# Kernel tuning notes

Hardware: AMD Instinct MI355X
Metric: run time of the kernel (lower is better)

## Reference

```python
import jax, jax.numpy as jnp
import numpy as np

B, S, D = 8, 4096, 512
BLOCK, LEFT, RIGHT = 64, 1, 1
FF = 2048
EPS = 1e-6


def setup_inputs() -> dict:
    key = jax.random.key(0)
    ks = jax.random.split(key, 16)
    sd = 1.0 / np.sqrt(D)
    sf = 1.0 / np.sqrt(FF)
    return {
        "x": jax.random.normal(ks[0], (B, S, D), jnp.float32),
        "Wq": jax.random.normal(ks[1], (D, D), jnp.float32) * sd,
        "bq": jnp.zeros((D,), jnp.float32),
        "Wk": jax.random.normal(ks[2], (D, D), jnp.float32) * sd,
        "bk": jnp.zeros((D,), jnp.float32),
        "Wv": jax.random.normal(ks[3], (D, D), jnp.float32) * sd,
        "bv": jnp.zeros((D,), jnp.float32),
        "W1": jax.random.normal(ks[4], (D, FF), jnp.float32) * sd,
        "b1": jnp.zeros((FF,), jnp.float32),
        "W2": jax.random.normal(ks[5], (FF, D), jnp.float32) * sf,
        "b2": jnp.zeros((D,), jnp.float32),
        "g1": jnp.ones((D,), jnp.float32),
        "be1": jnp.zeros((D,), jnp.float32),
        "g2": jnp.ones((D,), jnp.float32),
        "be2": jnp.zeros((D,), jnp.float32),
    }


def layernorm(x, g, b):
    m = jnp.mean(x, axis=-1, keepdims=True)
    v = jnp.mean(jnp.square(x - m), axis=-1, keepdims=True)
    return g * (x - m) * jax.lax.rsqrt(v + EPS) + b


def local_attention(x, Wq, bq, Wk, bk, Wv, bv):
    Bsz, Sl, Dm = x.shape
    nb = Sl // BLOCK          # number of blocks
    nw = LEFT + RIGHT + 1     # window (in blocks)
    q = (x @ Wq + bq).reshape(Bsz, nb, BLOCK, Dm)
    k = (x @ Wk + bk).reshape(Bsz, nb, BLOCK, Dm)
    v = (x @ Wv + bv).reshape(Bsz, nb, BLOCK, Dm)
    # pad block axis so every query block has LEFT/RIGHT neighbor blocks
    kp = jnp.pad(k, ((0, 0), (LEFT, RIGHT), (0, 0), (0, 0)))
    vp = jnp.pad(v, ((0, 0), (LEFT, RIGHT), (0, 0), (0, 0)))
    # gather windows: (B, nb, nw*BLOCK, D)
    k_win = jnp.stack([kp[:, j:j + nb] for j in range(nw)], axis=2).reshape(Bsz, nb, nw * BLOCK, Dm)
    v_win = jnp.stack([vp[:, j:j + nb] for j in range(nw)], axis=2).reshape(Bsz, nb, nw * BLOCK, Dm)
    # mask out-of-range (padded) blocks at sequence edges
    blk = jnp.arange(nb)[:, None] + jnp.arange(nw)[None, :] - LEFT  # (nb, nw)
    mask = ((blk >= 0) & (blk < nb))
    mask = jnp.repeat(mask, BLOCK, axis=1)  # (nb, nw*BLOCK)
    scores = jnp.einsum('bnqd,bnkd->bnqk', q, k_win) / jnp.sqrt(jnp.float32(Dm))
    scores = jnp.where(mask[None, :, None, :], scores, jnp.float32(-1e9))
    attn = jax.nn.softmax(scores, axis=-1)
    out = jnp.einsum('bnqk,bnkd->bnqd', attn, v_win)
    return out.reshape(Bsz, Sl, Dm)


def reference(x, Wq, bq, Wk, bk, Wv, bv, W1, b1, W2, b2, g1, be1, g2, be2):
    # inference mode: dropout is identity
    a = local_attention(x, Wq, bq, Wk, bk, Wv, bv)
    out1 = layernorm(x + a, g1, be1)
    ffn = jnp.maximum(out1 @ W1 + b1, 0.0) @ W2 + b2
    return layernorm(out1 + ffn, g2, be2)
```

## Files before the change

### kernel.cpp

```cpp
#include <hip/hip_runtime.h>


typedef __bf16 bf16;
typedef __bf16 bf16x8 __attribute__((ext_vector_type(8)));
typedef float  f32x4  __attribute__((ext_vector_type(4)));

#define DEV __device__ __forceinline__

#define BAR()  do { asm volatile("" ::: "memory"); __builtin_amdgcn_s_barrier(); asm volatile("" ::: "memory"); } while (0)
#define WAITV(n) asm volatile("s_waitcnt vmcnt(" #n ")" ::: "memory")
#define WAITV0() asm volatile("s_waitcnt vmcnt(0)" ::: "memory")

DEV void gload_lds16(const void* g, void* lds) {
  __builtin_amdgcn_global_load_lds(
      (const __attribute__((address_space(1))) void*)g,
      (__attribute__((address_space(3))) void*)lds, 16, 0, 0);
}

__global__ __launch_bounds__(256) void cast_to_bf16(const float* __restrict__ in,
                                                    bf16* __restrict__ out, int n8) {
  int i = blockIdx.x * 256 + threadIdx.x;
  if (i >= n8) return;
  float4 a0 = ((const float4*)in)[i * 2];
  float4 a1 = ((const float4*)in)[i * 2 + 1];
  bf16x8 o;
  o[0] = (bf16)a0.x; o[1] = (bf16)a0.y; o[2] = (bf16)a0.z; o[3] = (bf16)a0.w;
  o[4] = (bf16)a1.x; o[5] = (bf16)a1.y; o[6] = (bf16)a1.z; o[7] = (bf16)a1.w;
  ((bf16x8*)out)[i] = o;
}

__global__ __launch_bounds__(256) void transpose_cast(const float* __restrict__ W,
                                                      bf16* __restrict__ Wt, int K, int N) {
  __shared__ bf16 tile[64][66];
  const int n0 = blockIdx.x * 64, k0 = blockIdx.y * 64;
  const int t = threadIdx.x;
#pragma unroll
  for (int it = 0; it < 16; ++it) {
    int c = it * 256 + t;
    int kr = c >> 6, nc = c & 63;
    tile[nc][kr] = (bf16)W[(size_t)(k0 + kr) * N + n0 + nc];
  }
  __syncthreads();
#pragma unroll
  for (int it = 0; it < 2; ++it) {
    int c = it * 256 + t;
    int nr = c >> 3, kg = (c & 7) * 8;
    bf16x8 v;
#pragma unroll
    for (int e = 0; e < 8; ++e) v[e] = tile[nr][kg + e];
    *(bf16x8*)(Wt + (size_t)(n0 + nr) * K + k0 + kg) = v;
  }
}

__global__ __launch_bounds__(256) void concat_bias(const float* __restrict__ bq,
                                                   const float* __restrict__ bk,
                                                   const float* __restrict__ bv,
                                                   float* __restrict__ o) {
  int i = blockIdx.x * 256 + threadIdx.x;
  if (i < 512) o[i] = bq[i];
  else if (i < 1024) o[i] = bk[i - 512];
  else if (i < 1536) o[i] = bv[i - 1024];
}

template <int RELU, int F32OUT>
__global__ __launch_bounds__(512, 1)
void gemm256(const bf16* __restrict__ A, const bf16* __restrict__ Bt,
             const float* __restrict__ bias, void* __restrict__ Cout,
             int M, int N, int K) {
  __shared__ char LB[163840];
  const int tid = threadIdx.x;
  const int w = tid >> 6, l = tid & 63;
  const int lr = l & 15, lg = l >> 4;
  const int wm = w >> 2, wn = w & 3;

  const int bid = blockIdx.y * gridDim.x + blockIdx.x;
  const int NX = gridDim.y;
  const int xcd = bid & 7;
  const int idx = bid >> 3;
  const int mi = idx / NX;
  const int nn = idx - mi * NX;
  const int m0 = (xcd * 16 + mi) * 256;
  const int n0 = nn * 256;

  const int NT = K >> 6;

  int srow[4], scol[4];
#pragma unroll
  for (int j = 0; j < 4; ++j) {
    const int s = tid + 512 * j;
    srow[j] = s >> 3;
    scol[j] = (((s & 7) ^ ((s >> 3) & 7)) << 3);
  }

  const int swz0 = ((lg ^ (lr & 7)) << 4);
  const int swz1 = (((4 | lg) ^ (lr & 7)) << 4);

  f32x4 acc[8][4];
#pragma unroll
  for (int i = 0; i < 8; ++i)
#pragma unroll
    for (int j = 0; j < 4; ++j) acc[i][j] = f32x4{0.f, 0.f, 0.f, 0.f};

  auto stageA = [&](int t) {
    char* d = LB + (t % 3) * 32768 + tid * 16;
#pragma unroll
    for (int j = 0; j < 4; ++j)
      gload_lds16(A + (size_t)(m0 + srow[j]) * K + t * 64 + scol[j], d + j * 8192);
  };
  auto stageB = [&](int t) {
    char* d = LB + 98304 + (t & 1) * 32768 + tid * 16;
#pragma unroll
    for (int j = 0; j < 4; ++j)
      gload_lds16(Bt + (size_t)(n0 + srow[j]) * K + t * 64 + scol[j], d + j * 8192);
  };

  stageA(0); stageB(0); stageA(1);
  WAITV(4);
  BAR();

  for (int t = 0; t < NT; ++t) {
    if (t + 1 < NT) stageB(t + 1);
    if (t + 2 < NT) stageA(t + 2);
    const char* pA = LB + (t % 3) * 32768 + (wm << 14) + (lr << 7);
    const char* pB = LB + 98304 + (t & 1) * 32768 + (wn << 13) + (lr << 7);
    bf16x8 bv_[4][2];
#pragma unroll
    for (int n = 0; n < 4; ++n) {
      bv_[n][0] = *(const bf16x8*)(pB + n * 2048 + swz0);
      bv_[n][1] = *(const bf16x8*)(pB + n * 2048 + swz1);
    }
#pragma unroll
    for (int i = 0; i < 8; ++i) {
      bf16x8 a0 = *(const bf16x8*)(pA + i * 2048 + swz0);
      bf16x8 a1 = *(const bf16x8*)(pA + i * 2048 + swz1);
#pragma unroll
      for (int n = 0; n < 4; ++n) {
        acc[i][n] = __builtin_amdgcn_mfma_f32_16x16x32_bf16(a0, bv_[n][0], acc[i][n], 0, 0, 0);
        acc[i][n] = __builtin_amdgcn_mfma_f32_16x16x32_bf16(a1, bv_[n][1], acc[i][n], 0, 0, 0);
      }
    }
    if (t + 2 < NT) { WAITV(4); }
    else { WAITV0(); }
    BAR();
  }

  if (!F32OUT) {
    bf16* cl = (bf16*)LB;
    bf16* Cb = (bf16*)Cout;
#pragma unroll
    for (int half = 0; half < 2; ++half) {
      if (wm == half) {
#pragma unroll
        for (int n = 0; n < 4; ++n) {
          const int col = (wn << 6) + (n << 4) + lr;
          const float bv = bias[n0 + col];
#pragma unroll
          for (int m = 0; m < 8; ++m)
#pragma unroll
            for (int rg = 0; rg < 4; ++rg) {
              const int row = (m << 4) + (lg << 2) + rg;
              float v = acc[m][n][rg] + bv;
              if (RELU) v = fmaxf(v, 0.f);
              cl[row * 264 + col] = (bf16)v;
            }
        }
      }
      __syncthreads();
#pragma unroll
      for (int it = 0; it < 8; ++it) {
        const int idx2 = it * 512 + tid;
        const int r = idx2 >> 5, ch = idx2 & 31;
        *(bf16x8*)(Cb + (size_t)(m0 + half * 128 + r) * N + n0 + (ch << 3)) =
            *(const bf16x8*)(cl + r * 264 + (ch << 3));
      }
      __syncthreads();
    }
  } else {
    float* Cf = (float*)Cout;
#pragma unroll
    for (int n = 0; n < 4; ++n) {
      const int col = n0 + (wn << 6) + (n << 4) + lr;
      const float bv = bias[col];
#pragma unroll
      for (int m = 0; m < 8; ++m)
#pragma unroll
        for (int rg = 0; rg < 4; ++rg) {
          const int row = m0 + (wm << 7) + (m << 4) + (lg << 2) + rg;
          float v = acc[m][n][rg] + bv;
          if (RELU) v = fmaxf(v, 0.f);
          Cf[(size_t)row * N + col] = v;
        }
    }
  }
}

__global__ __launch_bounds__(256) void transpose_v(const bf16* __restrict__ qkv,
                                                   bf16* __restrict__ vt) {
  __shared__ bf16 tile[64][66];
  const int s0 = blockIdx.x * 64, d0 = blockIdx.y * 64, b = blockIdx.z;
  const int t = threadIdx.x;
#pragma unroll
  for (int it = 0; it < 2; ++it) {
    int c = it * 256 + t;
    int r = c >> 3, g = (c & 7) * 8;
    bf16x8 v = *(const bf16x8*)(qkv + ((size_t)b * 4096 + s0 + r) * 1536 + 1024 + d0 + g);
#pragma unroll
    for (int e = 0; e < 8; ++e) tile[g + e][r] = v[e];
  }
  __syncthreads();
#pragma unroll
  for (int it = 0; it < 2; ++it) {
    int c = it * 256 + t;
    int dr = c >> 3, sg = (c & 7) * 8;
    bf16x8 v;
#pragma unroll
    for (int e = 0; e < 8; ++e) v[e] = tile[dr][sg + e];
    *(bf16x8*)(vt + ((size_t)b * 512 + d0 + dr) * 4096 + s0 + sg) = v;
  }
}

__global__ __launch_bounds__(512, 4)
void attn_local(const bf16* __restrict__ qkv, const bf16* __restrict__ vt,
                bf16* __restrict__ aout) {
  __shared__ bf16 P[4][16][200];
  __shared__ float xmx[4][2][16];
  __shared__ float xsm[4][2][16];
  const int qb = blockIdx.x, b = blockIdx.y;
  const int t = threadIdx.x, w = t >> 6, l = t & 63;
  const int rg = w & 3, h = w >> 2;
  const int lr = l & 15, lg = l >> 4;

  bool val[6];
#pragma unroll
  for (int n = 0; n < 6; ++n) {
    int gn = 6 * h + n;
    val[n] = ((unsigned)(qb - 1 + (gn >> 2)) < 64u);
  }

  const size_t qrow = (size_t)b * 4096 + qb * 64 + rg * 16;
  const bf16* qp = qkv + (qrow + lr) * 1536 + lg * 8;
  const bf16* kbase = qkv + ((long)b * 4096 + (long)(qb - 1) * 64) * 1536 + 512;

  f32x4 S[6];
#pragma unroll
  for (int n = 0; n < 6; ++n) S[n] = f32x4{0.f, 0.f, 0.f, 0.f};

  for (int kk = 0; kk < 16; ++kk) {
    bf16x8 aq = *(const bf16x8*)(qp + kk * 32);
#pragma unroll
    for (int n = 0; n < 6; ++n) {
      if (!val[n]) continue;
      const int gn = 6 * h + n;
      bf16x8 bk = *(const bf16x8*)(kbase + (size_t)(gn * 16 + lr) * 1536 + kk * 32 + lg * 8);
      S[n] = __builtin_amdgcn_mfma_f32_16x16x32_bf16(aq, bk, S[n], 0, 0, 0);
    }
  }

  const float scale = 0.044194173824159216f;
  float mx[4] = {-3e38f, -3e38f, -3e38f, -3e38f};
#pragma unroll
  for (int n = 0; n < 6; ++n) {
    if (!val[n]) continue;
#pragma unroll
    for (int i = 0; i < 4; ++i) mx[i] = fmaxf(mx[i], S[n][i]);
  }
#pragma unroll
  for (int i = 0; i < 4; ++i) {
    mx[i] = fmaxf(mx[i], __shfl_xor(mx[i], 1));
    mx[i] = fmaxf(mx[i], __shfl_xor(mx[i], 2));
    mx[i] = fmaxf(mx[i], __shfl_xor(mx[i], 4));
    mx[i] = fmaxf(mx[i], __shfl_xor(mx[i], 8));
  }
  if (lr == 0) {
#pragma unroll
    for (int i = 0; i < 4; ++i) xmx[rg][h][lg * 4 + i] = mx[i];
  }
  __syncthreads();
  float m4[4];
#pragma unroll
  for (int i = 0; i < 4; ++i) m4[i] = fmaxf(mx[i], xmx[rg][h ^ 1][lg * 4 + i]);

  float sm[4] = {0.f, 0.f, 0.f, 0.f};
#pragma unroll
  for (int n = 0; n < 6; ++n) {
    if (!val[n]) continue;
#pragma unroll
    for (int i = 0; i < 4; ++i) {
      float p = __expf((S[n][i] - m4[i]) * scale);
      S[n][i] = p;
      sm[i] += p;
    }
  }
#pragma unroll
  for (int i = 0; i < 4; ++i) {
    sm[i] += __shfl_xor(sm[i], 1);
    sm[i] += __shfl_xor(sm[i], 2);
    sm[i] += __shfl_xor(sm[i], 4);
    sm[i] += __shfl_xor(sm[i], 8);
  }
  if (lr == 0) {
#pragma unroll
    for (int i = 0; i < 4; ++i) xsm[rg][h][lg * 4 + i] = sm[i];
  }
  __syncthreads();
  float rinv[4];
#pragma unroll
  for (int i = 0; i < 4; ++i) rinv[i] = 1.f / (sm[i] + xsm[rg][h ^ 1][lg * 4 + i]);

#pragma unroll
  for (int n = 0; n < 6; ++n) {
    const int gn = 6 * h + n;
#pragma unroll
    for (int i = 0; i < 4; ++i)
      P[rg][lg * 4 + i][gn * 16 + lr] = val[n] ? (bf16)(S[n][i] * rinv[i]) : (bf16)0.f;
  }
  __syncthreads();

  f32x4 O[4][4];
#pragma unroll
  for (int rt = 0; rt < 4; ++rt)
#pragma unroll
    for (int dt = 0; dt < 4; ++dt) O[rt][dt] = f32x4{0.f, 0.f, 0.f, 0.f};

  const bf16* vtb = vt + ((long)b * 512 + w * 64) * 4096 + (long)(qb - 1) * 64;
#pragma unroll
  for (int ks = 0; ks < 6; ++ks) {
    if ((unsigned)(qb - 1 + (ks >> 1)) >= 64u) continue;
    bf16x8 vf[4];
#pragma unroll
    for (int dt = 0; dt < 4; ++dt)
      vf[dt] = *(const bf16x8*)(vtb + (size_t)(dt * 16 + lr) * 4096 + ks * 32 + lg * 8);
#pragma unroll
    for (int rt = 0; rt < 4; ++rt) {
      bf16x8 pa = *(const bf16x8*)&P[rt][lr][ks * 32 + lg * 8];
#pragma unroll
      for (int dt = 0; dt < 4; ++dt)
        O[rt][dt] = __builtin_amdgcn_mfma_f32_16x16x32_bf16(pa, vf[dt], O[rt][dt], 0, 0, 0);
    }
  }

  const size_t orow = (size_t)b * 4096 + qb * 64;
#pragma unroll
  for (int rt = 0; rt < 4; ++rt)
#pragma unroll
    for (int dt = 0; dt < 4; ++dt)
#pragma unroll
      for (int i = 0; i < 4; ++i)
        aout[(orow + rt * 16 + lg * 4 + i) * 512 + w * 64 + dt * 16 + lr] =
            (bf16)O[rt][dt][i];
}

__global__ __launch_bounds__(256) void ln_res1(const float* __restrict__ x,
                                               const bf16* __restrict__ a,
                                               const float* __restrict__ g,
                                               const float* __restrict__ be,
                                               bf16* __restrict__ out) {
  const int t = threadIdx.x, w = t >> 6, l = t & 63;
  const size_t row = (size_t)blockIdx.x * 4 + w;
  const float* xp = x + row * 512 + l * 8;
  float4 x0 = ((const float4*)xp)[0];
  float4 x1 = ((const float4*)xp)[1];
  bf16x8 av = *(const bf16x8*)(a + row * 512 + l * 8);
  float s[8] = {x0.x + (float)av[0], x0.y + (float)av[1], x0.z + (float)av[2], x0.w + (float)av[3],
                x1.x + (float)av[4], x1.y + (float)av[5], x1.z + (float)av[6], x1.w + (float)av[7]};
  float sum = 0.f;
#pragma unroll
  for (int i = 0; i < 8; ++i) sum += s[i];
#pragma unroll
  for (int m = 1; m <= 32; m <<= 1) sum += __shfl_xor(sum, m);
  const float mean = sum * (1.f / 512.f);
  float vs = 0.f;
#pragma unroll
  for (int i = 0; i < 8; ++i) { float d = s[i] - mean; vs += d * d; }
#pragma unroll
  for (int m = 1; m <= 32; m <<= 1) vs += __shfl_xor(vs, m);
  const float r = rsqrtf(vs * (1.f / 512.f) + 1e-6f);
  float4 g0 = ((const float4*)(g + l * 8))[0], g1 = ((const float4*)(g + l * 8))[1];
  float4 b0 = ((const float4*)(be + l * 8))[0], b1 = ((const float4*)(be + l * 8))[1];
  bf16x8 o;
  o[0] = (bf16)(g0.x * (s[0] - mean) * r + b0.x);
  o[1] = (bf16)(g0.y * (s[1] - mean) * r + b0.y);
  o[2] = (bf16)(g0.z * (s[2] - mean) * r + b0.z);
  o[3] = (bf16)(g0.w * (s[3] - mean) * r + b0.w);
  o[4] = (bf16)(g1.x * (s[4] - mean) * r + b1.x);
  o[5] = (bf16)(g1.y * (s[5] - mean) * r + b1.y);
  o[6] = (bf16)(g1.z * (s[6] - mean) * r + b1.z);
  o[7] = (bf16)(g1.w * (s[7] - mean) * r + b1.w);
  *(bf16x8*)(out + row * 512 + l * 8) = o;
}

__global__ __launch_bounds__(256) void ln_res2(const bf16* __restrict__ o1,
                                               float* __restrict__ y,
                                               const float* __restrict__ g,
                                               const float* __restrict__ be) {
  const int t = threadIdx.x, w = t >> 6, l = t & 63;
  const size_t row = (size_t)blockIdx.x * 4 + w;
  float* yp = y + row * 512 + l * 8;
  float4 y0 = ((const float4*)yp)[0];
  float4 y1 = ((const float4*)yp)[1];
  bf16x8 ov = *(const bf16x8*)(o1 + row * 512 + l * 8);
  float s[8] = {y0.x + (float)ov[0], y0.y + (float)ov[1], y0.z + (float)ov[2], y0.w + (float)ov[3],
                y1.x + (float)ov[4], y1.y + (float)ov[5], y1.z + (float)ov[6], y1.w + (float)ov[7]};
  float sum = 0.f;
#pragma unroll
  for (int i = 0; i < 8; ++i) sum += s[i];
#pragma unroll
  for (int m = 1; m <= 32; m <<= 1) sum += __shfl_xor(sum, m);
  const float mean = sum * (1.f / 512.f);
  float vs = 0.f;
#pragma unroll
  for (int i = 0; i < 8; ++i) { float d = s[i] - mean; vs += d * d; }
#pragma unroll
  for (int m = 1; m <= 32; m <<= 1) vs += __shfl_xor(vs, m);
  const float r = rsqrtf(vs * (1.f / 512.f) + 1e-6f);
  float4 g0 = ((const float4*)(g + l * 8))[0], g1 = ((const float4*)(g + l * 8))[1];
  float4 b0 = ((const float4*)(be + l * 8))[0], b1 = ((const float4*)(be + l * 8))[1];
  float4 r0, r1;
  r0.x = g0.x * (s[0] - mean) * r + b0.x;
  r0.y = g0.y * (s[1] - mean) * r + b0.y;
  r0.z = g0.z * (s[2] - mean) * r + b0.z;
  r0.w = g0.w * (s[3] - mean) * r + b0.w;
  r1.x = g1.x * (s[4] - mean) * r + b1.x;
  r1.y = g1.y * (s[5] - mean) * r + b1.y;
  r1.z = g1.z * (s[6] - mean) * r + b1.z;
  r1.w = g1.w * (s[7] - mean) * r + b1.w;
  ((float4*)yp)[0] = r0;
  ((float4*)yp)[1] = r1;
}

extern "C" void kernel_launch(void* const* d_in, const int* in_sizes, int n_in,
                              void* d_out, int out_size, void* d_ws, size_t ws_size,
                              hipStream_t stream) {
  const float* x   = (const float*)d_in[0];
  const float* Wq  = (const float*)d_in[1];
  const float* bq  = (const float*)d_in[2];
  const float* Wk  = (const float*)d_in[3];
  const float* bk  = (const float*)d_in[4];
  const float* Wv  = (const float*)d_in[5];
  const float* bv  = (const float*)d_in[6];
  const float* W1  = (const float*)d_in[7];
  const float* b1  = (const float*)d_in[8];
  const float* W2  = (const float*)d_in[9];
  const float* b2  = (const float*)d_in[10];
  const float* g1  = (const float*)d_in[11];
  const float* be1 = (const float*)d_in[12];
  const float* g2  = (const float*)d_in[13];
  const float* be2 = (const float*)d_in[14];
  float* out = (float*)d_out;

  char* ws = (char*)d_ws;
  bf16*  WqkvT = (bf16*)(ws + 0);
  bf16*  W1T   = (bf16*)(ws + 1572864);
  bf16*  W2T   = (bf16*)(ws + 3670016);
  float* bqkv  = (float*)(ws + 5767168);
  bf16*  xb    = (bf16*)(ws + 6291456);
  bf16*  out1  = (bf16*)(ws + 39845888);
  bf16*  qkv   = (bf16*)(ws + 73400320);
  bf16*  vtb   = (bf16*)(ws + 174063616);
  bf16*  a_    = xb;
  bf16*  h     = qkv;

  cast_to_bf16<<<8192, 256, 0, stream>>>(x, xb, 2097152);
  transpose_cast<<<dim3(8, 8), 256, 0, stream>>>(Wq, WqkvT, 512, 512);
  transpose_cast<<<dim3(8, 8), 256, 0, stream>>>(Wk, WqkvT + 262144, 512, 512);
  transpose_cast<<<dim3(8, 8), 256, 0, stream>>>(Wv, WqkvT + 524288, 512, 512);
  transpose_cast<<<dim3(32, 8), 256, 0, stream>>>(W1, W1T, 512, 2048);
  transpose_cast<<<dim3(8, 32), 256, 0, stream>>>(W2, W2T, 2048, 512);
  concat_bias<<<6, 256, 0, stream>>>(bq, bk, bv, bqkv);

  gemm256<0, 0><<<dim3(128, 6), 512, 0, stream>>>(xb, WqkvT, bqkv, qkv, 32768, 1536, 512);
  transpose_v<<<dim3(64, 8, 8), 256, 0, stream>>>(qkv, vtb);
  attn_local<<<dim3(64, 8), 512, 0, stream>>>(qkv, vtb, a_);
  ln_res1<<<8192, 256, 0, stream>>>(x, a_, g1, be1, out1);
  gemm256<1, 0><<<dim3(128, 8), 512, 0, stream>>>(out1, W1T, b1, h, 32768, 2048, 512);
  gemm256<0, 1><<<dim3(128, 2), 512, 0, stream>>>(h, W2T, b2, out, 32768, 512, 2048);
  ln_res2<<<8192, 256, 0, stream>>>(out1, out, g2, be2);
}
```

Measured before the change: 397.0 us.

## Fuse weight prep, write V transposed from QKV GEMM, use bf16 residual paths

Merges the six weight transpose and bias-concat launches into one prep kernel. The QKV GEMM epilogue now writes V directly in transposed layout, so the separate transpose_v pass goes away. The second LayerNorm reads a bf16 FFN output instead of fp32, and the first residual reads bf16 x instead of fp32. This cuts launches and memory traffic, but the residual add now uses bf16-rounded x and FFN output, which costs some accuracy.

```diff
diff --git a/kernel.cpp b/kernel.cpp
--- a/kernel.cpp
+++ b/kernel.cpp
@@ -29,10 +29,8 @@
   ((bf16x8*)out)[i] = o;
 }
 
-__global__ __launch_bounds__(256) void transpose_cast(const float* __restrict__ W,
-                                                      bf16* __restrict__ Wt, int K, int N) {
-  __shared__ bf16 tile[64][66];
-  const int n0 = blockIdx.x * 64, k0 = blockIdx.y * 64;
+DEV void tc_body(const float* __restrict__ W, bf16* __restrict__ Wt,
+                 int K, int N, int n0, int k0, bf16 (*tile)[66]) {
   const int t = threadIdx.x;
 #pragma unroll
   for (int it = 0; it < 16; ++it) {
@@ -52,21 +50,40 @@
   }
 }
 
-__global__ __launch_bounds__(256) void concat_bias(const float* __restrict__ bq,
-                                                   const float* __restrict__ bk,
-                                                   const float* __restrict__ bv,
-                                                   float* __restrict__ o) {
-  int i = blockIdx.x * 256 + threadIdx.x;
-  if (i < 512) o[i] = bq[i];
-  else if (i < 1024) o[i] = bk[i - 512];
-  else if (i < 1536) o[i] = bv[i - 1024];
-}
-
-template <int RELU, int F32OUT>
+__global__ __launch_bounds__(256) void prep_weights(
+    const float* __restrict__ Wq, const float* __restrict__ Wk,
+    const float* __restrict__ Wv, const float* __restrict__ W1,
+    const float* __restrict__ W2, const float* __restrict__ bq,
+    const float* __restrict__ bk, const float* __restrict__ bv,
+    bf16* __restrict__ WqkvT, bf16* __restrict__ W1T, bf16* __restrict__ W2T,
+    float* __restrict__ bqkv) {
+  __shared__ bf16 tile[64][66];
+  const int bid = blockIdx.x;
+  if (bid < 192) {
+    const float* W = bid < 64 ? Wq : (bid < 128 ? Wk : Wv);
+    bf16* Wt = WqkvT + (size_t)(bid >> 6) * 262144;
+    const int t = bid & 63;
+    tc_body(W, Wt, 512, 512, (t & 7) * 64, (t >> 3) * 64, tile);
+  } else if (bid < 448) {
+    const int t = bid - 192;
+    tc_body(W1, W1T, 512, 2048, (t & 31) * 64, (t >> 5) * 64, tile);
+  } else if (bid < 704) {
+    const int t = bid - 448;
+    tc_body(W2, W2T, 2048, 512, (t & 7) * 64, (t >> 3) * 64, tile);
+  } else {
+    for (int i = threadIdx.x; i < 512; i += 256) {
+      bqkv[i] = bq[i];
+      bqkv[512 + i] = bk[i];
+      bqkv[1024 + i] = bv[i];
+    }
+  }
+}
+
+template <int RELU, int F32OUT, int VT>
 __global__ __launch_bounds__(512, 1)
 void gemm256(const bf16* __restrict__ A, const bf16* __restrict__ Bt,
              const float* __restrict__ bias, void* __restrict__ Cout,
-             int M, int N, int K) {
+             bf16* __restrict__ vt, int M, int N, int K) {
   __shared__ char LB[163840];
   const int tid = threadIdx.x;
   const int w = tid >> 6, l = tid & 63;
@@ -145,6 +162,7 @@
   }
 
   if (!F32OUT) {
+    const bool is_v = VT && (n0 >= 1024);
     bf16* cl = (bf16*)LB;
     bf16* Cb = (bf16*)Cout;
 #pragma unroll
@@ -166,12 +184,27 @@
         }
       }
       __syncthreads();
-#pragma unroll
-      for (int it = 0; it < 8; ++it) {
-        const int idx2 = it * 512 + tid;
-        const int r = idx2 >> 5, ch = idx2 & 31;
-        *(bf16x8*)(Cb + (size_t)(m0 + half * 128 + r) * N + n0 + (ch << 3)) =
-            *(const bf16x8*)(cl + r * 264 + (ch << 3));
+      if (!is_v) {
+#pragma unroll
+        for (int it = 0; it < 8; ++it) {
+          const int idx2 = it * 512 + tid;
+          const int r = idx2 >> 5, ch = idx2 & 31;
+          *(bf16x8*)(Cb + (size_t)(m0 + half * 128 + r) * N + n0 + (ch << 3)) =
+              *(const bf16x8*)(cl + r * 264 + (ch << 3));
+        }
+      } else {
+        const int b = m0 >> 12;
+        const int s0 = (m0 & 4095) + half * 128;
+        const int d0 = n0 - 1024;
+        const int d = tid >> 1, sc = (tid & 1) << 6;
+        bf16* dst = vt + ((size_t)b * 512 + d0 + d) * 4096 + s0 + sc;
+#pragma unroll
+        for (int c8 = 0; c8 < 8; ++c8) {
+          bf16x8 v;
+#pragma unroll
+          for (int e = 0; e < 8; ++e) v[e] = cl[(sc + c8 * 8 + e) * 264 + d];
+          *(bf16x8*)(dst + c8 * 8) = v;
+        }
       }
       __syncthreads();
     }
@@ -191,31 +224,6 @@
           Cf[(size_t)row * N + col] = v;
         }
     }
-  }
-}
-
-__global__ __launch_bounds__(256) void transpose_v(const bf16* __restrict__ qkv,
-                                                   bf16* __restrict__ vt) {
-  __shared__ bf16 tile[64][66];
-  const int s0 = blockIdx.x * 64, d0 = blockIdx.y * 64, b = blockIdx.z;
-  const int t = threadIdx.x;
-#pragma unroll
-  for (int it = 0; it < 2; ++it) {
-    int c = it * 256 + t;
-    int r = c >> 3, g = (c & 7) * 8;
-    bf16x8 v = *(const bf16x8*)(qkv + ((size_t)b * 4096 + s0 + r) * 1536 + 1024 + d0 + g);
-#pragma unroll
-    for (int e = 0; e < 8; ++e) tile[g + e][r] = v[e];
-  }
-  __syncthreads();
-#pragma unroll
-  for (int it = 0; it < 2; ++it) {
-    int c = it * 256 + t;
-    int dr = c >> 3, sg = (c & 7) * 8;
-    bf16x8 v;
-#pragma unroll
-    for (int e = 0; e < 8; ++e) v[e] = tile[dr][sg + e];
-    *(bf16x8*)(vt + ((size_t)b * 512 + d0 + dr) * 4096 + s0 + sg) = v;
   }
 }
 
@@ -350,19 +358,18 @@
             (bf16)O[rt][dt][i];
 }
 
-__global__ __launch_bounds__(256) void ln_res1(const float* __restrict__ x,
+__global__ __launch_bounds__(256) void ln_res1(const bf16* __restrict__ xb,
                                                const bf16* __restrict__ a,
                                                const float* __restrict__ g,
                                                const float* __restrict__ be,
                                                bf16* __restrict__ out) {
   const int t = threadIdx.x, w = t >> 6, l = t & 63;
   const size_t row = (size_t)blockIdx.x * 4 + w;
-  const float* xp = x + row * 512 + l * 8;
-  float4 x0 = ((const float4*)xp)[0];
-  float4 x1 = ((const float4*)xp)[1];
+  bf16x8 xv = *(const bf16x8*)(xb + row * 512 + l * 8);
   bf16x8 av = *(const bf16x8*)(a + row * 512 + l * 8);
-  float s[8] = {x0.x + (float)av[0], x0.y + (float)av[1], x0.z + (float)av[2], x0.w + (float)av[3],
-                x1.x + (float)av[4], x1.y + (float)av[5], x1.z + (float)av[6], x1.w + (float)av[7]};
+  float s[8];
+#pragma unroll
+  for (int i = 0; i < 8; ++i) s[i] = (float)xv[i] + (float)av[i];
   float sum = 0.f;
 #pragma unroll
   for (int i = 0; i < 8; ++i) sum += s[i];
@@ -389,18 +396,18 @@
   *(bf16x8*)(out + row * 512 + l * 8) = o;
 }
 
-__global__ __launch_bounds__(256) void ln_res2(const bf16* __restrict__ o1,
-                                               float* __restrict__ y,
-                                               const float* __restrict__ g,
-                                               const float* __restrict__ be) {
+__global__ __launch_bounds__(256) void ln_res2b(const bf16* __restrict__ o1,
+                                                const bf16* __restrict__ y2,
+                                                const float* __restrict__ g,
+                                                const float* __restrict__ be,
+                                                float* __restrict__ out) {
   const int t = threadIdx.x, w = t >> 6, l = t & 63;
   const size_t row = (size_t)blockIdx.x * 4 + w;
-  float* yp = y + row * 512 + l * 8;
-  float4 y0 = ((const float4*)yp)[0];
-  float4 y1 = ((const float4*)yp)[1];
   bf16x8 ov = *(const bf16x8*)(o1 + row * 512 + l * 8);
-  float s[8] = {y0.x + (float)ov[0], y0.y + (float)ov[1], y0.z + (float)ov[2], y0.w + (float)ov[3],
-                y1.x + (float)ov[4], y1.y + (float)ov[5], y1.z + (float)ov[6], y1.w + (float)ov[7]};
+  bf16x8 yv = *(const bf16x8*)(y2 + row * 512 + l * 8);
+  float s[8];
+#pragma unroll
+  for (int i = 0; i < 8; ++i) s[i] = (float)ov[i] + (float)yv[i];
   float sum = 0.f;
 #pragma unroll
   for (int i = 0; i < 8; ++i) sum += s[i];
@@ -424,6 +431,7 @@
   r1.y = g1.y * (s[5] - mean) * r + b1.y;
   r1.z = g1.z * (s[6] - mean) * r + b1.z;
   r1.w = g1.w * (s[7] - mean) * r + b1.w;
+  float* yp = out + row * 512 + l * 8;
   ((float4*)yp)[0] = r0;
   ((float4*)yp)[1] = r1;
 }
@@ -457,22 +465,21 @@
   bf16*  out1  = (bf16*)(ws + 39845888);
   bf16*  qkv   = (bf16*)(ws + 73400320);
   bf16*  vtb   = (bf16*)(ws + 174063616);
-  bf16*  a_    = xb;
+  bf16*  a_    = out1;
   bf16*  h     = qkv;
+  bf16*  y2    = xb;
 
   cast_to_bf16<<<8192, 256, 0, stream>>>(x, xb, 2097152);
-  transpose_cast<<<dim3(8, 8), 256, 0, stream>>>(Wq, WqkvT, 512, 512);
-  transpose_cast<<<dim3(8, 8), 256, 0, stream>>>(Wk, WqkvT + 262144, 512, 512);
-  transpose_cast<<<dim3(8, 8), 256, 0, stream>>>(Wv, WqkvT + 524288, 512, 512);
-  transpose_cast<<<dim3(32, 8), 256, 0, stream>>>(W1, W1T, 512, 2048);
-  transpose_cast<<<dim3(8, 32), 256, 0, stream>>>(W2, W2T, 2048, 512);
-  concat_bias<<<6, 256, 0, stream>>>(bq, bk, bv, bqkv);
-
-  gemm256<0, 0><<<dim3(128, 6), 512, 0, stream>>>(xb, WqkvT, bqkv, qkv, 32768, 1536, 512);
-  transpose_v<<<dim3(64, 8, 8), 256, 0, stream>>>(qkv, vtb);
+  prep_weights<<<705, 256, 0, stream>>>(Wq, Wk, Wv, W1, W2, bq, bk, bv,
+                                        WqkvT, W1T, W2T, bqkv);
+
+  gemm256<0, 0, 1><<<dim3(128, 6), 512, 0, stream>>>(xb, WqkvT, bqkv, qkv, vtb,
+                                                     32768, 1536, 512);
   attn_local<<<dim3(64, 8), 512, 0, stream>>>(qkv, vtb, a_);
-  ln_res1<<<8192, 256, 0, stream>>>(x, a_, g1, be1, out1);
-  gemm256<1, 0><<<dim3(128, 8), 512, 0, stream>>>(out1, W1T, b1, h, 32768, 2048, 512);
-  gemm256<0, 1><<<dim3(128, 2), 512, 0, stream>>>(h, W2T, b2, out, 32768, 512, 2048);
-  ln_res2<<<8192, 256, 0, stream>>>(out1, out, g2, be2);
-}
+  ln_res1<<<8192, 256, 0, stream>>>(xb, a_, g1, be1, out1);
+  gemm256<1, 0, 0><<<dim3(128, 8), 512, 0, stream>>>(out1, W1T, b1, h, nullptr,
+                                                     32768, 2048, 512);
+  gemm256<0, 0, 0><<<dim3(128, 2), 512, 0, stream>>>(h, W2T, b2, y2, nullptr,
+                                                     32768, 512, 2048);
+  ln_res2b<<<8192, 256, 0, stream>>>(out1, y2, g2, be2, out);
+}
```

Measured after the change: 366.9 us. 1.08x faster.
